# Kernel tuning notes

Measured on AMD Instinct MI355X. Metric: run time of the kernel, lower is better.

Reference implementation:

```python
import math
import jax, jax.numpy as jnp
import numpy as np

B, T, D, H = 2, 2048, 1024, 16  # batch, max_T, d_model, heads
DK = D // H


def setup_inputs() -> dict:
    key = jax.random.key(0)
    ks = jax.random.split(key, 5)
    scale = 1.0 / math.sqrt(D)
    return {
        "k": jax.random.normal(ks[0], (B, T, D), jnp.float32),
        "q": jax.random.normal(ks[1], (B, T, D), jnp.float32),
        "v": jax.random.normal(ks[2], (B, T, D), jnp.float32),
        "mask": jnp.ones((B, T), jnp.int32),
        "causal": 1,
        # Single shared Linear: the torch code binds the SAME nn.Linear to K/Q/V/out.
        "W": jax.random.uniform(ks[3], (D, D), jnp.float32, -scale, scale),
        "b": jax.random.uniform(ks[4], (D,), jnp.float32, -scale, scale),
    }


def reference(k, q, v, mask, causal, W, b):
    def proj(x):  # [B,T,D] -> [B,H,T,DK]
        return (x @ W.T + b).reshape(B, T, H, DK).transpose(0, 2, 1, 3)

    K, Q, V = proj(k), proj(q), proj(v)
    scores = jnp.einsum("bhqd,bhkd->bhqk", Q, K) / math.sqrt(DK)
    if causal:
        causal_mask = jnp.tril(jnp.ones((T, T), jnp.bool_))[None, None]
        scores = jnp.where(causal_mask, scores, -jnp.inf)
    # outer-product padding mask: [B,T] -> [B,1,T,T]
    m = mask.astype(jnp.float32)
    mm = (m[:, None, :, None] * m[:, None, None, :])  # [B,1,T,T]
    scores = jnp.where(mm == 0, -jnp.inf, scores)
    p = jax.nn.softmax(scores, axis=-1)  # dropout is identity in eval
    out = jnp.einsum("bhqk,bhkd->bhqd", p, V)  # [B,H,T,DK]
    concat = out.transpose(0, 2, 1, 3).reshape(B, T, D)
    return concat @ W.T + b
```

## Files before the change

### kernel.cpp

```cpp
#include <hip/hip_runtime.h>

#define TT 2048
#define DD 1024
#define HH 16
#define DKK 64
#define BB 2

typedef __attribute__((ext_vector_type(8))) short bf16x8;
typedef __attribute__((ext_vector_type(4))) short bf16x4;
typedef __attribute__((ext_vector_type(4))) float f32x4;
typedef __attribute__((ext_vector_type(4))) unsigned short us4;

__device__ __forceinline__ unsigned short f2bf(float f) {
  union { float f; unsigned int i; } v; v.f = f;
  unsigned int x = v.i;
  return (unsigned short)((x + 0x7fffu + ((x >> 16) & 1u)) >> 16);
}
__device__ __forceinline__ unsigned int cvtpk_bf16(float lo, float hi) {
  unsigned int r;
  asm("v_cvt_pk_bf16_f32 %0, %1, %2" : "=v"(r) : "v"(lo), "v"(hi));
  return r;
}
__device__ __forceinline__ void gload16(const void* g, void* l) {
  __builtin_amdgcn_global_load_lds((const __attribute__((address_space(1))) void*)g,
                                   (__attribute__((address_space(3))) void*)l,
                                   16, 0, 0);
}

#if defined(__has_builtin)
#if __has_builtin(__builtin_amdgcn_exp2f)
#define HAVE_EXP2 1
#endif
#if __has_builtin(__builtin_amdgcn_mfma_f32_16x16x16bf16_1k)
#define HAVE_MFMA16 1
#endif
#endif

__device__ __forceinline__ float fexp2(float x) {
#ifdef HAVE_EXP2
  return __builtin_amdgcn_exp2f(x);
#else
  return __builtin_exp2f(x);
#endif
}

__device__ __forceinline__ f32x4 mfma16(bf16x4 a, bf16x4 b, f32x4 c) {
#ifdef HAVE_MFMA16
  return __builtin_amdgcn_mfma_f32_16x16x16bf16_1k(a, b, c, 0, 0, 0);
#else
  asm volatile("v_mfma_f32_16x16x16_bf16 %0, %1, %2, %0\n\ts_nop 7\n\ts_nop 7"
               : "+v"(c) : "v"(a), "v"(b));
  return c;
#endif
}

__global__ __launch_bounds__(256)
void f2b_all(const float* __restrict__ k, const float* __restrict__ q,
             const float* __restrict__ v, const float* __restrict__ W,
             unsigned short* __restrict__ kb, unsigned short* __restrict__ qb,
             unsigned short* __restrict__ vb, unsigned short* __restrict__ Wb)
{
  const int n1 = (BB * TT * DD) / 4;
  const int nW = (DD * DD) / 4;
  const int total = 3 * n1 + nW;
  int i = blockIdx.x * 256 + threadIdx.x;
  const int stride = gridDim.x * 256;
  for (; i < total; i += stride) {
    const float* src; unsigned short* dst; int j = i;
    if (j < n1)            { src = k; dst = kb; }
    else if (j < 2 * n1)   { src = q; dst = qb; j -= n1; }
    else if (j < 3 * n1)   { src = v; dst = vb; j -= 2 * n1; }
    else                   { src = W; dst = Wb; j -= 3 * n1; }
    const float4 f = ((const float4*)src)[j];
    us4 o;
    o[0] = f2bf(f.x); o[1] = f2bf(f.y); o[2] = f2bf(f.z); o[3] = f2bf(f.w);
    ((us4*)dst)[j] = o;
  }
}


__global__ __launch_bounds__(256)
void gemm_proj(const unsigned short* __restrict__ kb, const unsigned short* __restrict__ qb,
               const unsigned short* __restrict__ vb, const unsigned short* __restrict__ W,
               const float* __restrict__ bias,
               unsigned short* __restrict__ Kp, unsigned short* __restrict__ Qp,
               unsigned short* __restrict__ Vt)
{
  __shared__ unsigned short lA[2][128 * 32];
  __shared__ unsigned short lB[2][128 * 32];
  const int tid = threadIdx.x;
  const int w = tid >> 6, l = tid & 63;
  const int hw = blockIdx.y * gridDim.x + blockIdx.x;
  const int virt = (hw & 7) * 96 + (hw >> 3);
  const int n0 = (virt & 7) * 128;
  const int my = virt >> 3;
  const int grp = my >> 5;
  const int m0 = (my & 31) * 128;
  const unsigned short* A = grp == 0 ? kb : (grp == 1 ? qb : vb);
  const int wr = w >> 1, wc = w & 1;
  const int lg = l >> 4, lc = l & 15;

  f32x4 acc[4][4];
#pragma unroll
  for (int i = 0; i < 4; ++i)
#pragma unroll
    for (int j = 0; j < 4; ++j) acc[i][j] = (f32x4){0.f, 0.f, 0.f, 0.f};

  const int scolb = (((l & 3) ^ ((l >> 2) & 3)) * 16);

  auto stage = [&](int buf, int k0) {
#pragma unroll
    for (int cc = 0; cc < 2; ++cc) {
      const int slot = w * 2 + cc;
      const int row = slot * 16 + (l >> 2);
      gload16(A + (size_t)(m0 + row) * DD + k0 + (scolb >> 1), &lA[buf][slot * 512]);
      gload16(W + (size_t)(n0 + row) * DD + k0 + (scolb >> 1), &lB[buf][slot * 512]);
    }
  };

  stage(0, 0);
  __syncthreads();
  int cur = 0;
#pragma unroll 1
  for (int kt = 0; kt < 32; ++kt) {
    if (kt < 31) stage(cur ^ 1, (kt + 1) * 32);
    const char* la = (const char*)lA[cur];
    const char* lb = (const char*)lB[cur];
    bf16x8 af[4], bfr[4];
#pragma unroll
    for (int mf = 0; mf < 4; ++mf)
      af[mf] = *(const bf16x8*)(la + (wr * 64 + mf * 16 + lc) * 64 + ((lg * 16) ^ ((lc & 3) << 4)));
#pragma unroll
    for (int nf = 0; nf < 4; ++nf)
      bfr[nf] = *(const bf16x8*)(lb + (wc * 64 + nf * 16 + lc) * 64 + ((lg * 16) ^ ((lc & 3) << 4)));
#pragma unroll
    for (int mf = 0; mf < 4; ++mf)
#pragma unroll
      for (int nf = 0; nf < 4; ++nf)
        acc[mf][nf] = __builtin_amdgcn_mfma_f32_16x16x32_bf16(af[mf], bfr[nf], acc[mf][nf], 0, 0, 0);
    __syncthreads();
    cur ^= 1;
  }

  const float scale = (grp == 1) ? 0.125f * 1.4426950408889634f : 1.0f;
#pragma unroll
  for (int nf = 0; nf < 4; ++nf) {
    const int colg = n0 + wc * 64 + nf * 16 + lc;
    const float bv = bias[colg];
#pragma unroll
    for (int mf = 0; mf < 4; ++mf) {
      const int rowg = m0 + wr * 64 + mf * 16 + lg * 4;
      if (grp < 2) {
        unsigned short* C = grp == 0 ? Kp : Qp;
#pragma unroll
        for (int r = 0; r < 4; ++r)
          C[(size_t)(rowg + r) * DD + colg] = f2bf(scale * (acc[mf][nf][r] + bv));
      } else {
        const int bb = rowg >> 11, t = rowg & (TT - 1);
        const int hh = colg >> 6, dk = colg & 63;
        us4 pk;
#pragma unroll
        for (int r = 0; r < 4; ++r) pk[r] = f2bf(acc[mf][nf][r] + bv);
        *(us4*)&Vt[((size_t)((bb * HH + hh) * DKK + dk)) * TT + t] = pk;
      }
    }
  }
}

__global__ __launch_bounds__(256)
void gemm_out(const unsigned short* __restrict__ A, const unsigned short* __restrict__ W,
              const float* __restrict__ bias, float* __restrict__ Cf)
{
  __shared__ unsigned short lA[2][128 * 32];
  __shared__ unsigned short lB[2][128 * 32];
  const int tid = threadIdx.x;
  const int w = tid >> 6, l = tid & 63;
  const int hw = blockIdx.y * gridDim.x + blockIdx.x;
  const int virt = (hw & 7) * 32 + (hw >> 3);
  const int n0 = (virt & 7) * 128, m0 = (virt >> 3) * 128;
  const int wr = w >> 1, wc = w & 1;
  const int lg = l >> 4, lc = l & 15;

  f32x4 acc[4][4];
#pragma unroll
  for (int i = 0; i < 4; ++i)
#pragma unroll
    for (int j = 0; j < 4; ++j) acc[i][j] = (f32x4){0.f, 0.f, 0.f, 0.f};

  const int scolb = (((l & 3) ^ ((l >> 2) & 3)) * 16);

  auto stage = [&](int buf, int k0) {
#pragma unroll
    for (int cc = 0; cc < 2; ++cc) {
      const int slot = w * 2 + cc;
      const int row = slot * 16 + (l >> 2);
      gload16(A + (size_t)(m0 + row) * DD + k0 + (scolb >> 1), &lA[buf][slot * 512]);
      gload16(W + (size_t)(n0 + row) * DD + k0 + (scolb >> 1), &lB[buf][slot * 512]);
    }
  };

  stage(0, 0);
  __syncthreads();
  int cur = 0;
#pragma unroll 1
  for (int kt = 0; kt < 32; ++kt) {
    if (kt < 31) stage(cur ^ 1, (kt + 1) * 32);
    const char* la = (const char*)lA[cur];
    const char* lb = (const char*)lB[cur];
    bf16x8 af[4], bfr[4];
#pragma unroll
    for (int mf = 0; mf < 4; ++mf)
      af[mf] = *(const bf16x8*)(la + (wr * 64 + mf * 16 + lc) * 64 + ((lg * 16) ^ ((lc & 3) << 4)));
#pragma unroll
    for (int nf = 0; nf < 4; ++nf)
      bfr[nf] = *(const bf16x8*)(lb + (wc * 64 + nf * 16 + lc) * 64 + ((lg * 16) ^ ((lc & 3) << 4)));
#pragma unroll
    for (int mf = 0; mf < 4; ++mf)
#pragma unroll
      for (int nf = 0; nf < 4; ++nf)
        acc[mf][nf] = __builtin_amdgcn_mfma_f32_16x16x32_bf16(af[mf], bfr[nf], acc[mf][nf], 0, 0, 0);
    __syncthreads();
    cur ^= 1;
  }

#pragma unroll
  for (int nf = 0; nf < 4; ++nf) {
    const int colg = n0 + wc * 64 + nf * 16 + lc;
    const float bv = bias[colg];
#pragma unroll
    for (int mf = 0; mf < 4; ++mf) {
      const int rowg = m0 + wr * 64 + mf * 16 + lg * 4;
#pragma unroll
      for (int r = 0; r < 4; ++r)
        Cf[(size_t)(rowg + r) * DD + colg] = acc[mf][nf][r] + bv;
    }
  }
}

__global__ __launch_bounds__(256)
void attn(const unsigned short* __restrict__ Qp,
          const unsigned short* __restrict__ Kp,
          const unsigned short* __restrict__ Vt,
          const int* __restrict__ maskp,
          const int* __restrict__ causalp,
          unsigned short* __restrict__ Oc)
{
  __shared__ unsigned short Kl[2][64 * 64];
  __shared__ unsigned short Vl[2][64 * 64];
  const int tid = threadIdx.x;
  const int w = tid >> 6, l = tid & 63;
  const int bh = blockIdx.x;
  const int qi = blockIdx.y;
  const int b = bh >> 4, h = bh & 15;
  const int lg = l >> 4, lc = l & 15;
  const int causal = causalp[0];

  const int swz = ((l & 7) ^ (l >> 3)) * 16;
  int kcoff[2], vcoff[4];
#pragma unroll
  for (int kk = 0; kk < 2; ++kk) kcoff[kk] = (kk * 64 + lg * 16) ^ ((lc & 7) << 4);
#pragma unroll
  for (int nfk = 0; nfk < 4; ++nfk) vcoff[nfk] = (nfk * 32 + lg * 8) ^ ((lc & 7) << 4);
  const int rowb = lc * 128;
  const int* mrow = maskp + b * TT;

  auto stage = [&](int buf, int c0) {
#pragma unroll
    for (int cc = 0; cc < 2; ++cc) {
      const int slot = w * 2 + cc;
      const int rr = slot * 8 + (l >> 3);
      gload16(Kp + (size_t)(b * TT + c0 + rr) * DD + h * DKK + (swz >> 1), &Kl[buf][slot * 512]);
      gload16(Vt + (size_t)((b * HH + h) * DKK + rr) * TT + c0 + (swz >> 1), &Vl[buf][slot * 512]);
    }
  };

#pragma unroll 1
  for (int part = 0; part < 2; ++part) {
    const int q0 = (part == 0 ? qi : 31 - qi) * 64;
    const int qr = q0 + w * 16 + lc;

    bf16x8 qf[2];
    {
      const unsigned short* qp = Qp + (size_t)(b * TT + qr) * DD + h * DKK + lg * 8;
      qf[0] = *(const bf16x8*)qp;
      qf[1] = *(const bf16x8*)(qp + 32);
    }
    f32x4 o[4];
#pragma unroll
    for (int nfo = 0; nfo < 4; ++nfo) o[nfo] = (f32x4){0.f, 0.f, 0.f, 0.f};
    float m = -1e30f, lsum = 0.f;

    const int ntiles = (causal ? (q0 + 64) : TT) >> 6;
    stage(0, 0);
    __syncthreads();
    int cur = 0;
#pragma unroll 1
    for (int t = 0; t < ntiles; ++t) {
      if (t + 1 < ntiles) stage(cur ^ 1, (t + 1) * 64);
      const int c0 = t * 64;
      const char* kl = (const char*)Kl[cur];
      const char* vl = (const char*)Vl[cur];

      f32x4 s[4];
#pragma unroll
      for (int nf = 0; nf < 4; ++nf) s[nf] = (f32x4){0.f, 0.f, 0.f, 0.f};
#pragma unroll
      for (int nf = 0; nf < 4; ++nf)
#pragma unroll
        for (int kk = 0; kk < 2; ++kk) {
          bf16x8 kf = *(const bf16x8*)(kl + rowb + kcoff[kk] + nf * 2048);
          s[nf] = __builtin_amdgcn_mfma_f32_16x16x32_bf16(kf, qf[kk], s[nf], 0, 0, 0);
        }

      const unsigned long long bal = __ballot(mrow[c0 + l] != 0);
      if (bal != ~0ull) {
#pragma unroll
        for (int nf = 0; nf < 4; ++nf) {
          const int4 mv = *(const int4*)&mrow[c0 + nf * 16 + lg * 4];
          const int mvr[4] = {mv.x, mv.y, mv.z, mv.w};
#pragma unroll
          for (int r = 0; r < 4; ++r)
            if (mvr[r] == 0) s[nf][r] = -1e30f;
        }
      }
      if (causal && (t == ntiles - 1)) {
#pragma unroll
        for (int nf = 0; nf < 4; ++nf)
#pragma unroll
          for (int r = 0; r < 4; ++r) {
            const int kg = c0 + nf * 16 + lg * 4 + r;
            if (kg > qr) s[nf][r] = -1e30f;
          }
      }

      float pm = fmaxf(fmaxf(fmaxf(s[0][0], s[0][1]), fmaxf(s[0][2], s[0][3])),
                       fmaxf(fmaxf(s[1][0], s[1][1]), fmaxf(s[1][2], s[1][3])));
      pm = fmaxf(pm, fmaxf(fmaxf(fmaxf(s[2][0], s[2][1]), fmaxf(s[2][2], s[2][3])),
                           fmaxf(fmaxf(s[3][0], s[3][1]), fmaxf(s[3][2], s[3][3]))));
      pm = fmaxf(pm, __shfl_xor(pm, 16, 64));
      pm = fmaxf(pm, __shfl_xor(pm, 32, 64));

      const float mn = fmaxf(fmaxf(m, pm), -1e28f);
      const float al = fexp2(m - mn);
      m = mn;
      float alr[4];
#pragma unroll
      for (int r = 0; r < 4; ++r) alr[r] = __shfl(al, lg * 4 + r, 64);
#pragma unroll
      for (int nfo = 0; nfo < 4; ++nfo)
#pragma unroll
        for (int r = 0; r < 4; ++r) o[nfo][r] *= alr[r];

      float ps = 0.f;
      bf16x4 pa[4];
#pragma unroll
      for (int nf = 0; nf < 4; ++nf) {
        const float p0 = fexp2(s[nf][0] - m);
        const float p1 = fexp2(s[nf][1] - m);
        const float p2 = fexp2(s[nf][2] - m);
        const float p3 = fexp2(s[nf][3] - m);
        ps += (p0 + p1) + (p2 + p3);
        union { unsigned int u[2]; bf16x4 v; } pk;
        pk.u[0] = cvtpk_bf16(p0, p1);
        pk.u[1] = cvtpk_bf16(p2, p3);
        pa[nf] = pk.v;
      }
      ps += __shfl_xor(ps, 16, 64);
      ps += __shfl_xor(ps, 32, 64);
      lsum = lsum * al + ps;

#pragma unroll
      for (int nfo = 0; nfo < 4; ++nfo)
#pragma unroll
        for (int nfk = 0; nfk < 4; ++nfk) {
          bf16x4 vb = *(const bf16x4*)(vl + rowb + vcoff[nfk] + nfo * 2048);
          o[nfo] = mfma16(pa[nfk], vb, o[nfo]);
        }

      __syncthreads();
      cur ^= 1;
    }

    float linv[4];
#pragma unroll
    for (int r = 0; r < 4; ++r) linv[r] = 1.0f / __shfl(lsum, lg * 4 + r, 64);
#pragma unroll
    for (int nfo = 0; nfo < 4; ++nfo) {
      const int dg = h * DKK + nfo * 16 + lc;
#pragma unroll
      for (int r = 0; r < 4; ++r) {
        const int qg = q0 + w * 16 + lg * 4 + r;
        Oc[(size_t)(b * TT + qg) * DD + dg] = f2bf(o[nfo][r] * linv[r]);
      }
    }
  }
}

extern "C" void kernel_launch(void* const* d_in, const int* in_sizes, int n_in,
                              void* d_out, int out_size, void* d_ws, size_t ws_size,
                              hipStream_t stream)
{
  (void)in_sizes; (void)n_in; (void)out_size; (void)ws_size;
  const float* kf = (const float*)d_in[0];
  const float* qf = (const float*)d_in[1];
  const float* vf = (const float*)d_in[2];
  const int* mask = (const int*)d_in[3];
  const int* causal = (const int*)d_in[4];
  const float* Wf = (const float*)d_in[5];
  const float* bf = (const float*)d_in[6];

  const size_t MB = 1024 * 1024;
  char* ws = (char*)d_ws;
  unsigned short* kb = (unsigned short*)(ws);
  unsigned short* qb = (unsigned short*)(ws + 8 * MB);
  unsigned short* vb = (unsigned short*)(ws + 16 * MB);
  unsigned short* Wb = (unsigned short*)(ws + 24 * MB);
  unsigned short* Kp = (unsigned short*)(ws + 26 * MB);
  unsigned short* Qp = (unsigned short*)(ws + 34 * MB);
  unsigned short* Vt = (unsigned short*)(ws + 42 * MB);
  unsigned short* Oc = kb;

  f2b_all<<<dim3(2048), dim3(256), 0, stream>>>(kf, qf, vf, Wf, kb, qb, vb, Wb);
  gemm_proj<<<dim3(8, 96), dim3(256), 0, stream>>>(kb, qb, vb, Wb, bf, Kp, Qp, Vt);
  attn<<<dim3(32, 16), dim3(256), 0, stream>>>(Qp, Kp, Vt, mask, causal, Oc);
  gemm_out<<<dim3(8, 32), dim3(256), 0, stream>>>(Oc, Wb, bf, (float*)d_out);
}
```

Baseline: 138.4 us.

## Process paired causal query tiles in one shared KV loop

The attention kernel now handles both of its query tiles (qi and 31-qi) in a single pass over K/V tiles instead of two sequential passes. Each staged K/V tile in LDS is used by both query blocks, so the shorter block's K/V loads are no longer repeated and there is one fewer pipeline warm-up. The cost is roughly double the accumulator and score registers, which may lower occupancy, plus predicated MFMA and softmax work for the inactive block in later iterations.

```diff
diff --git a/kernel.cpp b/kernel.cpp
--- a/kernel.cpp
+++ b/kernel.cpp
@@ -255,6 +255,30 @@
   const int lg = l >> 4, lc = l & 15;
   const int causal = causalp[0];
 
+  const int q0a = qi * 64;
+  const int q0b = (31 - qi) * 64;
+  const int n0 = causal ? (qi + 1) : (TT >> 6);
+  const int n1 = causal ? (32 - qi) : (TT >> 6);
+  const int qra = q0a + w * 16 + lc;
+  const int qrb = q0b + w * 16 + lc;
+
+  bf16x8 qfa[2], qfb[2];
+  {
+    const unsigned short* qp = Qp + (size_t)(b * TT + qra) * DD + h * DKK + lg * 8;
+    qfa[0] = *(const bf16x8*)qp;
+    qfa[1] = *(const bf16x8*)(qp + 32);
+    const unsigned short* qp2 = Qp + (size_t)(b * TT + qrb) * DD + h * DKK + lg * 8;
+    qfb[0] = *(const bf16x8*)qp2;
+    qfb[1] = *(const bf16x8*)(qp2 + 32);
+  }
+  f32x4 oa[4], ob[4];
+#pragma unroll
+  for (int nfo = 0; nfo < 4; ++nfo) {
+    oa[nfo] = (f32x4){0.f, 0.f, 0.f, 0.f};
+    ob[nfo] = (f32x4){0.f, 0.f, 0.f, 0.f};
+  }
+  float ma = -1e30f, la = 0.f, mb = -1e30f, lb_ = 0.f;
+
   const int swz = ((l & 7) ^ (l >> 3)) * 16;
   int kcoff[2], vcoff[4];
 #pragma unroll
@@ -274,123 +298,140 @@
     }
   };
 
+  auto softmax = [&](f32x4 (&s)[4], float& m, float& lsum, bf16x4 (&pa)[4],
+                     f32x4 (&o)[4]) {
+    float pm = fmaxf(fmaxf(fmaxf(s[0][0], s[0][1]), fmaxf(s[0][2], s[0][3])),
+                     fmaxf(fmaxf(s[1][0], s[1][1]), fmaxf(s[1][2], s[1][3])));
+    pm = fmaxf(pm, fmaxf(fmaxf(fmaxf(s[2][0], s[2][1]), fmaxf(s[2][2], s[2][3])),
+                         fmaxf(fmaxf(s[3][0], s[3][1]), fmaxf(s[3][2], s[3][3]))));
+    pm = fmaxf(pm, __shfl_xor(pm, 16, 64));
+    pm = fmaxf(pm, __shfl_xor(pm, 32, 64));
+    const float mn = fmaxf(fmaxf(m, pm), -1e28f);
+    const float al = fexp2(m - mn);
+    m = mn;
+    float alr[4];
+#pragma unroll
+    for (int r = 0; r < 4; ++r) alr[r] = __shfl(al, lg * 4 + r, 64);
+#pragma unroll
+    for (int nfo = 0; nfo < 4; ++nfo)
+#pragma unroll
+      for (int r = 0; r < 4; ++r) o[nfo][r] *= alr[r];
+    float ps = 0.f;
+#pragma unroll
+    for (int nf = 0; nf < 4; ++nf) {
+      const float p0 = fexp2(s[nf][0] - m);
+      const float p1 = fexp2(s[nf][1] - m);
+      const float p2 = fexp2(s[nf][2] - m);
+      const float p3 = fexp2(s[nf][3] - m);
+      ps += (p0 + p1) + (p2 + p3);
+      union { unsigned int u[2]; bf16x4 v; } pk;
+      pk.u[0] = cvtpk_bf16(p0, p1);
+      pk.u[1] = cvtpk_bf16(p2, p3);
+      pa[nf] = pk.v;
+    }
+    ps += __shfl_xor(ps, 16, 64);
+    ps += __shfl_xor(ps, 32, 64);
+    lsum = lsum * al + ps;
+  };
+
+  stage(0, 0);
+  __syncthreads();
+  int cur = 0;
 #pragma unroll 1
-  for (int part = 0; part < 2; ++part) {
-    const int q0 = (part == 0 ? qi : 31 - qi) * 64;
-    const int qr = q0 + w * 16 + lc;
-
-    bf16x8 qf[2];
-    {
-      const unsigned short* qp = Qp + (size_t)(b * TT + qr) * DD + h * DKK + lg * 8;
-      qf[0] = *(const bf16x8*)qp;
-      qf[1] = *(const bf16x8*)(qp + 32);
-    }
-    f32x4 o[4];
-#pragma unroll
-    for (int nfo = 0; nfo < 4; ++nfo) o[nfo] = (f32x4){0.f, 0.f, 0.f, 0.f};
-    float m = -1e30f, lsum = 0.f;
-
-    const int ntiles = (causal ? (q0 + 64) : TT) >> 6;
-    stage(0, 0);
+  for (int t = 0; t < n1; ++t) {
+    if (t + 1 < n1) stage(cur ^ 1, (t + 1) * 64);
+    const int c0 = t * 64;
+    const char* kl = (const char*)Kl[cur];
+    const char* vl = (const char*)Vl[cur];
+    const bool act0 = (t < n0);
+
+    f32x4 sa[4], sb[4];
+#pragma unroll
+    for (int nf = 0; nf < 4; ++nf) {
+      sa[nf] = (f32x4){0.f, 0.f, 0.f, 0.f};
+      sb[nf] = (f32x4){0.f, 0.f, 0.f, 0.f};
+    }
+#pragma unroll
+    for (int nf = 0; nf < 4; ++nf)
+#pragma unroll
+      for (int kk = 0; kk < 2; ++kk) {
+        bf16x8 kf = *(const bf16x8*)(kl + rowb + kcoff[kk] + nf * 2048);
+        if (act0) sa[nf] = __builtin_amdgcn_mfma_f32_16x16x32_bf16(kf, qfa[kk], sa[nf], 0, 0, 0);
+        sb[nf] = __builtin_amdgcn_mfma_f32_16x16x32_bf16(kf, qfb[kk], sb[nf], 0, 0, 0);
+      }
+
+    const unsigned long long bal = __ballot(mrow[c0 + l] != 0);
+    if (bal != ~0ull) {
+#pragma unroll
+      for (int nf = 0; nf < 4; ++nf) {
+        const int4 mv = *(const int4*)&mrow[c0 + nf * 16 + lg * 4];
+        const int mvr[4] = {mv.x, mv.y, mv.z, mv.w};
+#pragma unroll
+        for (int r = 0; r < 4; ++r)
+          if (mvr[r] == 0) { sa[nf][r] = -1e30f; sb[nf][r] = -1e30f; }
+      }
+    }
+    if (causal && act0 && (t == n0 - 1)) {
+#pragma unroll
+      for (int nf = 0; nf < 4; ++nf)
+#pragma unroll
+        for (int r = 0; r < 4; ++r) {
+          const int kg = c0 + nf * 16 + lg * 4 + r;
+          if (kg > qra) sa[nf][r] = -1e30f;
+        }
+    }
+    if (causal && (t == n1 - 1)) {
+#pragma unroll
+      for (int nf = 0; nf < 4; ++nf)
+#pragma unroll
+        for (int r = 0; r < 4; ++r) {
+          const int kg = c0 + nf * 16 + lg * 4 + r;
+          if (kg > qrb) sb[nf][r] = -1e30f;
+        }
+    }
+
+    bf16x4 paa[4], pab[4];
+    if (act0) softmax(sa, ma, la, paa, oa);
+    softmax(sb, mb, lb_, pab, ob);
+
+#pragma unroll
+    for (int nfo = 0; nfo < 4; ++nfo)
+#pragma unroll
+      for (int nfk = 0; nfk < 4; ++nfk) {
+        bf16x4 vb = *(const bf16x4*)(vl + rowb + vcoff[nfk] + nfo * 2048);
+        if (act0) oa[nfo] = mfma16(paa[nfk], vb, oa[nfo]);
+        ob[nfo] = mfma16(pab[nfk], vb, ob[nfo]);
+      }
+
     __syncthreads();
-    int cur = 0;
-#pragma unroll 1
-    for (int t = 0; t < ntiles; ++t) {
-      if (t + 1 < ntiles) stage(cur ^ 1, (t + 1) * 64);
-      const int c0 = t * 64;
-      const char* kl = (const char*)Kl[cur];
-      const char* vl = (const char*)Vl[cur];
-
-      f32x4 s[4];
-#pragma unroll
-      for (int nf = 0; nf < 4; ++nf) s[nf] = (f32x4){0.f, 0.f, 0.f, 0.f};
-#pragma unroll
-      for (int nf = 0; nf < 4; ++nf)
-#pragma unroll
-        for (int kk = 0; kk < 2; ++kk) {
-          bf16x8 kf = *(const bf16x8*)(kl + rowb + kcoff[kk] + nf * 2048);
-          s[nf] = __builtin_amdgcn_mfma_f32_16x16x32_bf16(kf, qf[kk], s[nf], 0, 0, 0);
-        }
-
-      const unsigned long long bal = __ballot(mrow[c0 + l] != 0);
-      if (bal != ~0ull) {
-#pragma unroll
-        for (int nf = 0; nf < 4; ++nf) {
-          const int4 mv = *(const int4*)&mrow[c0 + nf * 16 + lg * 4];
-          const int mvr[4] = {mv.x, mv.y, mv.z, mv.w};
-#pragma unroll
-          for (int r = 0; r < 4; ++r)
-            if (mvr[r] == 0) s[nf][r] = -1e30f;
-        }
-      }
-      if (causal && (t == ntiles - 1)) {
-#pragma unroll
-        for (int nf = 0; nf < 4; ++nf)
-#pragma unroll
-          for (int r = 0; r < 4; ++r) {
-            const int kg = c0 + nf * 16 + lg * 4 + r;
-            if (kg > qr) s[nf][r] = -1e30f;
-          }
-      }
-
-      float pm = fmaxf(fmaxf(fmaxf(s[0][0], s[0][1]), fmaxf(s[0][2], s[0][3])),
-                       fmaxf(fmaxf(s[1][0], s[1][1]), fmaxf(s[1][2], s[1][3])));
-      pm = fmaxf(pm, fmaxf(fmaxf(fmaxf(s[2][0], s[2][1]), fmaxf(s[2][2], s[2][3])),
-                           fmaxf(fmaxf(s[3][0], s[3][1]), fmaxf(s[3][2], s[3][3]))));
-      pm = fmaxf(pm, __shfl_xor(pm, 16, 64));
-      pm = fmaxf(pm, __shfl_xor(pm, 32, 64));
-
-      const float mn = fmaxf(fmaxf(m, pm), -1e28f);
-      const float al = fexp2(m - mn);
-      m = mn;
-      float alr[4];
-#pragma unroll
-      for (int r = 0; r < 4; ++r) alr[r] = __shfl(al, lg * 4 + r, 64);
-#pragma unroll
-      for (int nfo = 0; nfo < 4; ++nfo)
-#pragma unroll
-        for (int r = 0; r < 4; ++r) o[nfo][r] *= alr[r];
-
-      float ps = 0.f;
-      bf16x4 pa[4];
-#pragma unroll
-      for (int nf = 0; nf < 4; ++nf) {
-        const float p0 = fexp2(s[nf][0] - m);
-        const float p1 = fexp2(s[nf][1] - m);
-        const float p2 = fexp2(s[nf][2] - m);
-        const float p3 = fexp2(s[nf][3] - m);
-        ps += (p0 + p1) + (p2 + p3);
-        union { unsigned int u[2]; bf16x4 v; } pk;
-        pk.u[0] = cvtpk_bf16(p0, p1);
-        pk.u[1] = cvtpk_bf16(p2, p3);
-        pa[nf] = pk.v;
-      }
-      ps += __shfl_xor(ps, 16, 64);
-      ps += __shfl_xor(ps, 32, 64);
-      lsum = lsum * al + ps;
-
-#pragma unroll
-      for (int nfo = 0; nfo < 4; ++nfo)
-#pragma unroll
-        for (int nfk = 0; nfk < 4; ++nfk) {
-          bf16x4 vb = *(const bf16x4*)(vl + rowb + vcoff[nfk] + nfo * 2048);
-          o[nfo] = mfma16(pa[nfk], vb, o[nfo]);
-        }
-
-      __syncthreads();
-      cur ^= 1;
-    }
-
+    cur ^= 1;
+  }
+
+  {
     float linv[4];
 #pragma unroll
-    for (int r = 0; r < 4; ++r) linv[r] = 1.0f / __shfl(lsum, lg * 4 + r, 64);
+    for (int r = 0; r < 4; ++r) linv[r] = 1.0f / __shfl(la, lg * 4 + r, 64);
 #pragma unroll
     for (int nfo = 0; nfo < 4; ++nfo) {
       const int dg = h * DKK + nfo * 16 + lc;
 #pragma unroll
       for (int r = 0; r < 4; ++r) {
-        const int qg = q0 + w * 16 + lg * 4 + r;
-        Oc[(size_t)(b * TT + qg) * DD + dg] = f2bf(o[nfo][r] * linv[r]);
+        const int qg = q0a + w * 16 + lg * 4 + r;
+        Oc[(size_t)(b * TT + qg) * DD + dg] = f2bf(oa[nfo][r] * linv[r]);
+      }
+    }
+  }
+  {
+    float linv[4];
+#pragma unroll
+    for (int r = 0; r < 4; ++r) linv[r] = 1.0f / __shfl(lb_, lg * 4 + r, 64);
+#pragma unroll
+    for (int nfo = 0; nfo < 4; ++nfo) {
+      const int dg = h * DKK + nfo * 16 + lc;
+#pragma unroll
+      for (int r = 0; r < 4; ++r) {
+        const int qg = q0b + w * 16 + lg * 4 + r;
+        Oc[(size_t)(b * TT + qg) * DD + dg] = f2bf(ob[nfo][r] * linv[r]);
       }
     }
   }
```

Result: slower. 153.6 us (+11.0%).
